# Kernel optimization log

Measured on AMD Instinct MI355X. Metric: run time of the kernel, lower is better.

## Reference

```python
import jax, jax.numpy as jnp
import numpy as np

N_EMBD = 2048
N_HEAD = 32
HEAD_SIZE = 64          # n_embd // n_head
MIX_DIM = 64            # RWKV-6 time-mix LoRA dim
DECAY_DIM = 128         # RWKV-6 decay LoRA dim
BATCH = 1024
STATE_ROWS = (2 + HEAD_SIZE) * 1  # single block, i = 0


def setup_inputs() -> dict:
    key = jax.random.key(0)
    ks = jax.random.split(key, 32)
    rn = lambda k, shp, s=0.02: jax.random.normal(k, shp, jnp.float32) * s
    d = {}
    d['x'] = jax.random.normal(ks[0], (BATCH, N_EMBD), jnp.float32)
    d['state'] = jax.random.normal(ks[1], (BATCH, STATE_ROWS, N_EMBD), jnp.float32) * 0.1
    d['ln1_w'] = jnp.ones((N_EMBD,), jnp.float32)
    d['ln1_b'] = jnp.zeros((N_EMBD,), jnp.float32)
    d['ln2_w'] = jnp.ones((N_EMBD,), jnp.float32)
    d['ln2_b'] = jnp.zeros((N_EMBD,), jnp.float32)
    d['maa_x'] = rn(ks[2], (N_EMBD,), 0.1)
    d['maa_w'] = rn(ks[3], (N_EMBD,), 0.1)
    d['maa_k'] = rn(ks[4], (N_EMBD,), 0.1)
    d['maa_v'] = rn(ks[5], (N_EMBD,), 0.1)
    d['maa_r'] = rn(ks[6], (N_EMBD,), 0.1)
    d['maa_g'] = rn(ks[7], (N_EMBD,), 0.1)
    d['maa_w1'] = rn(ks[8], (N_EMBD, 5 * MIX_DIM))
    d['maa_w2'] = rn(ks[9], (5, MIX_DIM, N_EMBD))
    d['decay'] = rn(ks[10], (N_EMBD,), 0.5) - 4.0  # typical negative log-decay
    d['decay_w1'] = rn(ks[11], (N_EMBD, DECAY_DIM))
    d['decay_w2'] = rn(ks[12], (DECAY_DIM, N_EMBD))
    d['faaaa'] = rn(ks[13], (N_HEAD, HEAD_SIZE, 1), 0.1)
    d['Wr'] = rn(ks[14], (N_EMBD, N_EMBD))
    d['Wk'] = rn(ks[15], (N_EMBD, N_EMBD))
    d['Wv'] = rn(ks[16], (N_EMBD, N_EMBD))
    d['Wo'] = rn(ks[17], (N_EMBD, N_EMBD))
    d['Wg'] = rn(ks[18], (N_EMBD, N_EMBD))
    d['gn_w'] = jnp.ones((N_EMBD,), jnp.float32)
    d['gn_b'] = jnp.zeros((N_EMBD,), jnp.float32)
    d['ffn_maa_k'] = rn(ks[19], (N_EMBD,), 0.1)
    d['ffn_maa_r'] = rn(ks[20], (N_EMBD,), 0.1)
    d['ffn_Wk'] = rn(ks[21], (N_EMBD, N_EMBD))
    d['ffn_Wr'] = rn(ks[22], (N_EMBD, N_EMBD))
    d['ffn_Wv'] = rn(ks[23], (N_EMBD, N_EMBD))
    d['i'] = 0
    return d


def _ln(x, w, b):
    mu = jnp.mean(x, -1, keepdims=True)
    var = jnp.var(x, -1, keepdims=True)
    return (x - mu) * jax.lax.rsqrt(var + 1e-5) * w + b


def reference(x, state, ln1_w, ln1_b, ln2_w, ln2_b,
              maa_x, maa_w, maa_k, maa_v, maa_r, maa_g, maa_w1, maa_w2,
              decay, decay_w1, decay_w2, faaaa,
              Wr, Wk, Wv, Wo, Wg, gn_w, gn_b,
              ffn_maa_k, ffn_maa_r, ffn_Wk, ffn_Wr, ffn_Wv, i):
    B = x.shape[0]
    H, S = N_HEAD, HEAD_SIZE
    # ---------------- time mixing ----------------
    xn = _ln(x, ln1_w, ln1_b)
    i1 = (2 + S) * i + 1
    sx = state[:, i1] - xn                                  # token shift delta
    xxx = xn + sx * maa_x
    xxx = jnp.tanh(xxx @ maa_w1).reshape(B, 5, 1, MIX_DIM)
    xxx = jnp.matmul(xxx, maa_w2).reshape(B, 5, N_EMBD)     # [B,5,E]
    mw, mk, mv, mr, mg = (xxx[:, j] for j in range(5))
    xw = xn + sx * (maa_w + mw)
    xk = xn + sx * (maa_k + mk)
    xv = xn + sx * (maa_v + mv)
    xr = xn + sx * (maa_r + mr)
    xg = xn + sx * (maa_g + mg)
    w = decay + jnp.tanh(xw @ decay_w1) @ decay_w2          # [B,E]
    w = jnp.exp(-jnp.exp(w.reshape(B, H, S, 1)))            # decay gate
    r = (xr @ Wr.T).reshape(B, H, 1, S)
    k = (xk @ Wk.T).reshape(B, H, S, 1)
    v = (xv @ Wv.T).reshape(B, H, 1, S)
    g = jax.nn.silu(xg @ Wg.T)
    s = state[:, (2 + S) * i + 2:(2 + S) * (i + 1), :].reshape(B, H, S, S)
    a = jnp.matmul(k, v)                                    # [B,H,S,S] outer product
    y = jnp.matmul(r, faaaa * a + s).reshape(B, N_EMBD)     # wkv readout
    # group norm (n_head groups over n_embd channels)
    yg = y.reshape(B, H, S)
    mu = jnp.mean(yg, -1, keepdims=True)
    var = jnp.var(yg, -1, keepdims=True)
    yg = ((yg - mu) * jax.lax.rsqrt(var + 1e-5)).reshape(B, N_EMBD) * gn_w + gn_b
    x1 = x + (yg * g) @ Wo.T
    # ---------------- channel mixing ----------------
    xn2 = _ln(x1, ln2_w, ln2_b)
    i0 = (2 + S) * i
    sx2 = state[:, i0] - xn2
    xk2 = xn2 + sx2 * ffn_maa_k
    xr2 = xn2 + sx2 * ffn_maa_r
    rr = jax.nn.sigmoid(xr2 @ ffn_Wr.T)
    kk = jnp.square(jax.nn.relu(xk2 @ ffn_Wk.T))
    return x1 + rr * (kk @ ffn_Wv.T)
```

## Files before the change

kernel.cpp:

```cpp
#include <hip/hip_runtime.h>
#include <cstdint>
#include <cstddef>

typedef unsigned short u16;
typedef __attribute__((ext_vector_type(8))) short bf16x8;
typedef __attribute__((ext_vector_type(4))) float f32x4;

#define DEV __device__ __forceinline__

DEV u16 f2bf(float f) {
  uint32_t b = __float_as_uint(f);
  b += 0x7fffu + ((b >> 16) & 1u);
  return (u16)(b >> 16);
}
DEV float bf2f(u16 u) { return __uint_as_float(((uint32_t)u) << 16); }

DEV void gl16(const u16* g, u16* l) {
  __builtin_amdgcn_global_load_lds(
      (const __attribute__((address_space(1))) void*)g,
      (__attribute__((address_space(3))) void*)l, 16, 0, 0);
}

struct CvtArgs { const float* s[8]; };

__global__ __launch_bounds__(256) void k_cvt_ln(
    const float* __restrict__ w1, const float* __restrict__ w2,
    u16* __restrict__ w1t, u16* __restrict__ w2t,
    const float* __restrict__ x, const float* __restrict__ state,
    const int* __restrict__ ip,
    const float* __restrict__ lw, const float* __restrict__ lb,
    const float* __restrict__ mx,
    u16* __restrict__ xn_o, u16* __restrict__ sx_o, u16* __restrict__ a1_o) {
  __shared__ float ls1[4], ls2[4];
  if (blockIdx.x < 4608) {
    int idx = blockIdx.x * 256 + threadIdx.x;
    if (idx < 655360) {
      int n = idx >> 11, k = idx & 2047;
      w1t[idx] = f2bf(w1[(size_t)k * 320 + n]);
    } else {
      int r = idx - 655360;
      int j = r >> 17, q = r & 131071;
      int n = q >> 6, k2 = q & 63;
      w2t[r] = f2bf(w2[((size_t)(j + 1) * 64 + k2) * 2048 + n]);
    }
  } else {
    int b = blockIdx.x - 4608, t = threadIdx.x;
    const float* xr = x + (size_t)b * 2048;
    float4 v0 = *(const float4*)(xr + t * 8);
    float4 v1 = *(const float4*)(xr + t * 8 + 4);
    float xv[8] = {v0.x, v0.y, v0.z, v0.w, v1.x, v1.y, v1.z, v1.w};
    float s1 = 0.f, s2 = 0.f;
#pragma unroll
    for (int j = 0; j < 8; ++j) { s1 += xv[j]; s2 += xv[j] * xv[j]; }
#pragma unroll
    for (int off = 32; off; off >>= 1) { s1 += __shfl_xor(s1, off); s2 += __shfl_xor(s2, off); }
    int w = t >> 6;
    if ((t & 63) == 0) { ls1[w] = s1; ls2[w] = s2; }
    __syncthreads();
    s1 = ls1[0] + ls1[1] + ls1[2] + ls1[3];
    s2 = ls2[0] + ls2[1] + ls2[2] + ls2[3];
    float mu = s1 * (1.0f / 2048.0f);
    float var = s2 * (1.0f / 2048.0f) - mu * mu;
    float rs = rsqrtf(var + 1e-5f);
    const float* st = state + ((size_t)b * 66 + (size_t)66 * ip[0] + 1) * 2048;
    int e0 = t * 8;
    uint4 xnp, sxp, a1p;
    u16* xnl = (u16*)&xnp; u16* sxl = (u16*)&sxp; u16* a1l = (u16*)&a1p;
#pragma unroll
    for (int j = 0; j < 8; ++j) {
      int e = e0 + j;
      float xn = (xv[j] - mu) * rs * lw[e] + lb[e];
      float sxv = st[e] - xn;
      xnl[j] = f2bf(xn); sxl[j] = f2bf(sxv); a1l[j] = f2bf(xn + sxv * mx[e]);
    }
    size_t o = (size_t)b * 2048 + e0;
    *(uint4*)(xn_o + o) = xnp;
    *(uint4*)(sx_o + o) = sxp;
    *(uint4*)(a1_o + o) = a1p;
  }
}

__global__ __launch_bounds__(256) void k_tanhpack(const float* __restrict__ p2,
                                                  u16* __restrict__ xb) {
  int idx = blockIdx.x * 256 + threadIdx.x;
  float s = p2[idx] + p2[327680 + idx] + p2[2 * 327680 + idx] + p2[3 * 327680 + idx];
  xb[idx] = f2bf(tanhf(s));
}

__global__ __launch_bounds__(256) void k_act(const u16* __restrict__ p8,
                                             u16* __restrict__ rr, u16* __restrict__ kk) {
  const size_t S = 2097152;
  int gid = blockIdx.x * 256 + threadIdx.x;
  size_t e0 = (size_t)(gid & 262143) * 8;
  int isk = gid >= 262144;
  const u16* base = p8 + (isk ? 4 * S : 0) + e0;
  float acc[8] = {};
#pragma unroll
  for (int s = 0; s < 4; ++s) {
    uint4 v = *(const uint4*)(base + (size_t)s * S);
    u16* vl = (u16*)&v;
#pragma unroll
    for (int j = 0; j < 8; ++j) acc[j] += bf2f(vl[j]);
  }
  uint4 p; u16* pl = (u16*)&p;
  if (!isk) {
#pragma unroll
    for (int j = 0; j < 8; ++j) pl[j] = f2bf(1.f / (1.f + __expf(-acc[j])));
    *(uint4*)(rr + e0) = p;
  } else {
#pragma unroll
    for (int j = 0; j < 8; ++j) { float r = acc[j] > 0.f ? acc[j] : 0.f; pl[j] = f2bf(r * r); }
    *(uint4*)(kk + e0) = p;
  }
}

__global__ __launch_bounds__(256) void k_fin(const u16* __restrict__ x1b,
                                             const u16* __restrict__ p9,
                                             const u16* __restrict__ rr,
                                             float* __restrict__ out) {
  const size_t S = 2097152;
  size_t e0 = ((size_t)blockIdx.x * 256 + threadIdx.x) * 8;
  float acc[8] = {};
#pragma unroll
  for (int s = 0; s < 4; ++s) {
    uint4 v = *(const uint4*)(p9 + (size_t)s * S + e0);
    u16* vl = (u16*)&v;
#pragma unroll
    for (int j = 0; j < 8; ++j) acc[j] += bf2f(vl[j]);
  }
  uint4 xv4 = *(const uint4*)(x1b + e0); u16* xl = (u16*)&xv4;
  uint4 rv = *(const uint4*)(rr + e0); u16* rl = (u16*)&rv;
  float o[8];
#pragma unroll
  for (int j = 0; j < 8; ++j) o[j] = bf2f(xl[j]) + bf2f(rl[j]) * acc[j];
  *(float4*)(out + e0) = make_float4(o[0], o[1], o[2], o[3]);
  *(float4*)(out + e0 + 4) = make_float4(o[4], o[5], o[6], o[7]);
}

__global__ __launch_bounds__(256) void k_ln_mix2(
    const float* __restrict__ x, const u16* __restrict__ p6,
    const float* __restrict__ state, const int* __restrict__ ip,
    const float* __restrict__ lw, const float* __restrict__ lb,
    const float* __restrict__ mk, const float* __restrict__ mr,
    u16* __restrict__ xk_o, u16* __restrict__ xr_o, u16* __restrict__ x1b_o) {
  const size_t S = 2097152;
  int b = blockIdx.x, t = threadIdx.x;
  size_t off = (size_t)b * 2048 + t * 8;
  float4 v0 = *(const float4*)(x + off);
  float4 v1 = *(const float4*)(x + off + 4);
  float xv[8] = {v0.x, v0.y, v0.z, v0.w, v1.x, v1.y, v1.z, v1.w};
#pragma unroll
  for (int s = 0; s < 4; ++s) {
    uint4 v = *(const uint4*)(p6 + (size_t)s * S + off);
    u16* vl = (u16*)&v;
#pragma unroll
    for (int j = 0; j < 8; ++j) xv[j] += bf2f(vl[j]);
  }
  uint4 x1p; u16* x1l = (u16*)&x1p;
#pragma unroll
  for (int j = 0; j < 8; ++j) x1l[j] = f2bf(xv[j]);
  *(uint4*)(x1b_o + off) = x1p;
  float s1 = 0.f, s2 = 0.f;
#pragma unroll
  for (int j = 0; j < 8; ++j) { s1 += xv[j]; s2 += xv[j] * xv[j]; }
#pragma unroll
  for (int off2 = 32; off2; off2 >>= 1) { s1 += __shfl_xor(s1, off2); s2 += __shfl_xor(s2, off2); }
  __shared__ float ls1[4], ls2[4];
  int w = t >> 6;
  if ((t & 63) == 0) { ls1[w] = s1; ls2[w] = s2; }
  __syncthreads();
  s1 = ls1[0] + ls1[1] + ls1[2] + ls1[3];
  s2 = ls2[0] + ls2[1] + ls2[2] + ls2[3];
  float mu = s1 * (1.0f / 2048.0f);
  float var = s2 * (1.0f / 2048.0f) - mu * mu;
  float rs = rsqrtf(var + 1e-5f);
  const float* st = state + ((size_t)b * 66 + (size_t)66 * ip[0] + 0) * 2048;
  int e0 = t * 8;
  uint4 xkp, xrp;
  u16* xkl = (u16*)&xkp; u16* xrl = (u16*)&xrp;
#pragma unroll
  for (int j = 0; j < 8; ++j) {
    int e = e0 + j;
    float xn = (xv[j] - mu) * rs * lw[e] + lb[e];
    float sxv = st[e] - xn;
    xkl[j] = f2bf(xn + sxv * mk[e]);
    xrl[j] = f2bf(xn + sxv * mr[e]);
  }
  *(uint4*)(xk_o + off) = xkp;
  *(uint4*)(xr_o + off) = xrp;
}

enum { EP_STORE = 0, EP_SILU, EP_MIX, EP_STOREF };

struct GemmDesc {
  const u16* A; const u16* B; void* C;
  const void* p1; const void* p2; const float* pvec;
  int lda, ldb, ldc, N, K, k0, ep;
};
struct GemmBatch { GemmDesc g[8]; int bpg; };

__global__ __launch_bounds__(256, 3) void k_gemmc(GemmBatch bat, int ngemm,
                                                  CvtArgs ca, u16* __restrict__ cdst,
                                                  int cvtoff) {
  if (blockIdx.x >= ngemm) {
    size_t idx = ((size_t)(blockIdx.x - ngemm + cvtoff) * 256 + threadIdx.x) * 8;
    int w = (int)(idx >> 22);
    size_t off = idx & ((1u << 22) - 1);
    const float* s = ca.s[w];
    float4 v0 = *(const float4*)(s + off);
    float4 v1 = *(const float4*)(s + off + 4);
    uint4 p; u16* pl = (u16*)&p;
    pl[0] = f2bf(v0.x); pl[1] = f2bf(v0.y); pl[2] = f2bf(v0.z); pl[3] = f2bf(v0.w);
    pl[4] = f2bf(v1.x); pl[5] = f2bf(v1.y); pl[6] = f2bf(v1.z); pl[7] = f2bf(v1.w);
    *(uint4*)(cdst + ((size_t)w << 22) + off) = p;
    return;
  }
  int gi = blockIdx.x / bat.bpg;
  int bid = blockIdx.x % bat.bpg;
  GemmDesc g = bat.g[gi];
  int ntn = (g.N + 127) >> 7;
  int m0 = (bid / ntn) << 7;
  int n0 = (bid % ntn) << 7;
  __shared__ u16 As[2][128 * 32];
  __shared__ u16 Bs[2][128 * 32];
  int t = threadIdx.x, w = t >> 6, lane = t & 63;
  int wm = w >> 1, wn = w & 1;
  int lr = lane & 15, kb = (lane >> 4) * 8;
  const u16* Ab = g.A + (size_t)(m0 + w * 32 + (lane >> 2)) * g.lda + (lane & 3) * 8;
  const u16* Bb = g.B + (size_t)(n0 + w * 32 + (lane >> 2)) * g.ldb + (lane & 3) * 8;
  int a16 = 16 * g.lda, b16 = 16 * g.ldb;
  int aoff = (w * 32) * 32;
  f32x4 acc[4][4] = {};
  int nt = g.K >> 5;

  auto stage = [&](int buf, int kk) {
    u16* Ad = (u16*)As + buf * 4096 + aoff;
    u16* Bd = (u16*)Bs + buf * 4096 + aoff;
    gl16(Ab + kk, Ad);
    gl16(Ab + kk + a16, Ad + 512);
    gl16(Bb + kk, Bd);
    gl16(Bb + kk + b16, Bd + 512);
  };

  stage(0, g.k0);
  __syncthreads();
  int cur = 0;
  for (int ti = 0; ti < nt; ++ti) {
    if (ti + 1 < nt) stage(cur ^ 1, g.k0 + (ti + 1) * 32);
    const u16* Ac = (const u16*)As + cur * 4096;
    const u16* Bc = (const u16*)Bs + cur * 4096;
    bf16x8 af[4], bfr[4];
#pragma unroll
    for (int m = 0; m < 4; ++m)
      af[m] = *(const bf16x8*)(Ac + (wm * 64 + m * 16 + lr) * 32 + kb);
#pragma unroll
    for (int n = 0; n < 4; ++n)
      bfr[n] = *(const bf16x8*)(Bc + (wn * 64 + n * 16 + lr) * 32 + kb);
#pragma unroll
    for (int m = 0; m < 4; ++m)
#pragma unroll
      for (int n = 0; n < 4; ++n)
        acc[m][n] = __builtin_amdgcn_mfma_f32_16x16x32_bf16(af[m], bfr[n], acc[m][n], 0, 0, 0);
    __syncthreads();
    cur ^= 1;
  }

  int ep = g.ep;
#pragma unroll
  for (int m = 0; m < 4; ++m) {
    int grow0 = m0 + wm * 64 + m * 16 + (lane >> 4) * 4;
#pragma unroll
    for (int n = 0; n < 4; ++n) {
      int gc = n0 + wn * 64 + n * 16 + lr;
      if (gc >= g.N) continue;
#pragma unroll
      for (int q = 0; q < 4; ++q) {
        size_t ci = (size_t)(grow0 + q) * g.ldc + gc;
        float v = acc[m][n][q];
        switch (ep) {
          case EP_STORE: ((u16*)g.C)[ci] = f2bf(v); break;
          case EP_MIX: {
            float xn = bf2f(((const u16*)g.p1)[ci]);
            float sxv = bf2f(((const u16*)g.p2)[ci]);
            ((u16*)g.C)[ci] = f2bf(xn + sxv * (g.pvec[gc] + v));
          } break;
          case EP_STOREF: ((float*)g.C)[ci] = v; break;
          default: break;
        }
      }
    }
  }
}

__global__ __launch_bounds__(512, 2) void k_gemm2(GemmBatch bat) {
  extern __shared__ u16 lds[];
  int nwg = gridDim.x;
  int wg0 = blockIdx.x;
  int wg = (wg0 & 7) * (nwg >> 3) + (wg0 >> 3);
  int gi = wg / bat.bpg;
  int bid = wg % bat.bpg;
  GemmDesc g = bat.g[gi];
  int ntn = (g.N + 255) >> 8;
  int m0 = (bid / ntn) << 7;
  int n0 = (bid % ntn) << 8;
  int t = threadIdx.x, wv = t >> 6, lane = t & 63;
  int wm = wv >> 2, wn = wv & 3;
  int lr = lane & 15, hi = lane >> 4;

  const u16* asrc[2]; const u16* bsrc[4];
#pragma unroll
  for (int j = 0; j < 2; ++j) {
    int cid = t + 512 * j, r = cid >> 3, c = cid & 7;
    asrc[j] = g.A + (size_t)(m0 + r) * g.lda + ((c ^ (r & 7)) << 3);
  }
#pragma unroll
  for (int j = 0; j < 4; ++j) {
    int cid = t + 512 * j, r = cid >> 3, c = cid & 7;
    bsrc[j] = g.B + (size_t)(n0 + r) * g.ldb + ((c ^ (r & 7)) << 3);
  }
  int au = wv * 512;

  auto stage = [&](int buf, int k) {
    u16* base = lds + buf * 24576;
#pragma unroll
    for (int j = 0; j < 2; ++j) gl16(asrc[j] + k, base + au + j * 4096);
#pragma unroll
    for (int j = 0; j < 4; ++j) gl16(bsrc[j] + k, base + 8192 + au + j * 4096);
  };

  int arow[4], brow[4];
#pragma unroll
  for (int m = 0; m < 4; ++m) arow[m] = wm * 64 + m * 16 + lr;
#pragma unroll
  for (int n = 0; n < 4; ++n) brow[n] = wn * 64 + n * 16 + lr;

  f32x4 acc[4][4] = {};
  int nt = g.K >> 6;
  stage(0, g.k0);
  if (nt > 1) stage(1, g.k0 + 64);

  for (int ti = 0; ti < nt; ++ti) {
    if (ti + 1 < nt) asm volatile("s_waitcnt vmcnt(6)" ::: "memory");
    else             asm volatile("s_waitcnt vmcnt(0)" ::: "memory");
    __builtin_amdgcn_sched_barrier(0);
    __builtin_amdgcn_s_barrier();
    __builtin_amdgcn_sched_barrier(0);
    const u16* buf = lds + (ti % 3) * 24576;
    bf16x8 af[4][2], bf[4][2];
#pragma unroll
    for (int m = 0; m < 4; ++m)
#pragma unroll
      for (int ks = 0; ks < 2; ++ks)
        af[m][ks] = *(const bf16x8*)(buf + arow[m] * 64 + ((((ks << 2) + hi) ^ (arow[m] & 7)) << 3));
#pragma unroll
    for (int n = 0; n < 4; ++n)
#pragma unroll
      for (int ks = 0; ks < 2; ++ks)
        bf[n][ks] = *(const bf16x8*)(buf + 8192 + brow[n] * 64 + ((((ks << 2) + hi) ^ (brow[n] & 7)) << 3));
    if (ti + 2 < nt) stage((ti + 2) % 3, g.k0 + (ti + 2) * 64);
    __builtin_amdgcn_s_setprio(1);
#pragma unroll
    for (int m = 0; m < 4; ++m)
#pragma unroll
      for (int n = 0; n < 4; ++n)
#pragma unroll
        for (int ks = 0; ks < 2; ++ks)
          acc[m][n] = __builtin_amdgcn_mfma_f32_16x16x32_bf16(af[m][ks], bf[n][ks], acc[m][n], 0, 0, 0);
    __builtin_amdgcn_s_setprio(0);
  }

  int ep = g.ep;
#pragma unroll
  for (int m = 0; m < 4; ++m) {
    int grow0 = m0 + wm * 64 + m * 16 + hi * 4;
#pragma unroll
    for (int n = 0; n < 4; ++n) {
      int gc = n0 + wn * 64 + n * 16 + lr;
#pragma unroll
      for (int q = 0; q < 4; ++q) {
        size_t ci = (size_t)(grow0 + q) * g.ldc + gc;
        float v = acc[m][n][q];
        switch (ep) {
          case EP_STORE: ((u16*)g.C)[ci] = f2bf(v); break;
          case EP_SILU:  ((u16*)g.C)[ci] = f2bf(v / (1.f + __expf(-v))); break;
          case EP_STOREF: ((float*)g.C)[ci] = v; break;
          default: break;
        }
      }
    }
  }
}

__global__ __launch_bounds__(512, 2) void k_gemm3(GemmBatch bat) {
  extern __shared__ u16 lds[];
  int nwg = gridDim.x;
  int wg0 = blockIdx.x;
  int wg = (wg0 & 7) * (nwg >> 3) + (wg0 >> 3);
  GemmDesc g = bat.g[wg / bat.bpg];
  int bid = wg % bat.bpg;
  int ntn = g.N >> 8;
  int m0 = (bid / ntn) << 8;
  int n0 = (bid % ntn) << 8;
  int t = threadIdx.x, wv = t >> 6, lane = t & 63;
  int wm = wv >> 2, wn = wv & 3;
  int lr = lane & 15, hi = lane >> 4;

  const u16* asrc[4]; const u16* bsrc[4];
#pragma unroll
  for (int j = 0; j < 4; ++j) {
    int cid = t + 512 * j, r = cid >> 3, c = cid & 7;
    asrc[j] = g.A + (size_t)(m0 + r) * g.lda + ((c ^ (r & 7)) << 3);
    bsrc[j] = g.B + (size_t)(n0 + r) * g.ldb + ((c ^ (r & 7)) << 3);
  }
  int au = wv * 512;

  auto stage = [&](int buf, int k) {
    u16* ab = lds + buf * 32768 + au;
    u16* bb = lds + buf * 32768 + 16384 + au;
#pragma unroll
    for (int j = 0; j < 4; ++j) gl16(asrc[j] + k, ab + j * 4096);
#pragma unroll
    for (int j = 0; j < 4; ++j) gl16(bsrc[j] + k, bb + j * 4096);
  };

  int arow[8], brow[4];
#pragma unroll
  for (int m = 0; m < 8; ++m) arow[m] = wm * 128 + m * 16 + lr;
#pragma unroll
  for (int n = 0; n < 4; ++n) brow[n] = wn * 64 + n * 16 + lr;

  f32x4 acc[8][4] = {};
  int nt = g.K >> 6;
  stage(0, g.k0);
  if (nt > 1) stage(1, g.k0 + 64);

  for (int ti = 0; ti < nt; ++ti) {
    if (ti + 1 < nt) asm volatile("s_waitcnt vmcnt(8)" ::: "memory");
    else             asm volatile("s_waitcnt vmcnt(0)" ::: "memory");
    __builtin_amdgcn_sched_barrier(0);
    __builtin_amdgcn_s_barrier();
    __builtin_amdgcn_sched_barrier(0);
    const u16* buf = lds + (ti & 1) * 32768;
#pragma unroll
    for (int ks = 0; ks < 2; ++ks) {
      bf16x8 af[8], bf[4];
#pragma unroll
      for (int m = 0; m < 8; ++m)
        af[m] = *(const bf16x8*)(buf + arow[m] * 64 + ((((ks << 2) + hi) ^ (arow[m] & 7)) << 3));
#pragma unroll
      for (int n = 0; n < 4; ++n)
        bf[n] = *(const bf16x8*)(buf + 16384 + brow[n] * 64 + ((((ks << 2) + hi) ^ (brow[n] & 7)) << 3));
      __builtin_amdgcn_s_setprio(1);
#pragma unroll
      for (int m = 0; m < 8; ++m)
#pragma unroll
        for (int n = 0; n < 4; ++n)
          acc[m][n] = __builtin_amdgcn_mfma_f32_16x16x32_bf16(af[m], bf[n], acc[m][n], 0, 0, 0);
      __builtin_amdgcn_s_setprio(0);
    }
    __builtin_amdgcn_sched_barrier(0);
    __builtin_amdgcn_s_barrier();
    __builtin_amdgcn_sched_barrier(0);
    if (ti + 2 < nt) stage(ti & 1, g.k0 + (ti + 2) * 64);
  }

#pragma unroll
  for (int m = 0; m < 8; ++m) {
    int grow0 = m0 + wm * 128 + m * 16 + hi * 4;
#pragma unroll
    for (int n = 0; n < 4; ++n) {
      int gc = n0 + wn * 64 + n * 16 + lr;
#pragma unroll
      for (int q = 0; q < 4; ++q)
        ((u16*)g.C)[(size_t)(grow0 + q) * g.ldc + gc] = f2bf(acc[m][n][q]);
    }
  }
}

__global__ __launch_bounds__(256) void k_wkv(
    const u16* __restrict__ p4,
    const float* __restrict__ state, const int* __restrict__ ip,
    const float* __restrict__ fa, const float* __restrict__ gw,
    const float* __restrict__ gbias, u16* __restrict__ t_o) {
  const size_t S = 2097152;
  int t = threadIdx.x, w = t >> 6, lane = t & 63;
  int flat = blockIdx.x * 4 + w;
  int b = flat >> 5, h = flat & 31;
  size_t base = ((size_t)b << 11) + (h << 6) + lane;
  float r  = bf2f(p4[base])         + bf2f(p4[S + base]);
  float kv = bf2f(p4[2 * S + base]) + bf2f(p4[3 * S + base]);
  float vv = bf2f(p4[4 * S + base]) + bf2f(p4[5 * S + base]);
  float gs = bf2f(p4[6 * S + base]) + bf2f(p4[7 * S + base]);
  float gg = gs / (1.f + __expf(-gs));
  float f  = fa[(h << 6) + lane];
  __shared__ float rs[4][64];
  rs[w][lane] = r;
  __syncthreads();
  float c = r * f * kv;
#pragma unroll
  for (int off = 32; off; off >>= 1) c += __shfl_xor(c, off);

  const float* sp = state + ((size_t)b * 66 + (size_t)66 * ip[0] + 2 + 2 * h) * 2048;
  int q = lane >> 4, jj = lane & 15;
  float yp0 = 0.f, yp1 = 0.f, yp2 = 0.f, yp3 = 0.f;
#pragma unroll
  for (int ib = 0; ib < 16; ++ib) {
    int i = ib * 4 + q;
    float4 sv = *(const float4*)(sp + ((i >> 5) * 2048) + ((i & 31) << 6) + jj * 4);
    float ri = rs[w][i];
    yp0 += ri * sv.x; yp1 += ri * sv.y; yp2 += ri * sv.z; yp3 += ri * sv.w;
  }
#pragma unroll
  for (int off = 16; off <= 32; off <<= 1) {
    yp0 += __shfl_xor(yp0, off); yp1 += __shfl_xor(yp1, off);
    yp2 += __shfl_xor(yp2, off); yp3 += __shfl_xor(yp3, off);
  }
  int src = lane >> 2, cc = lane & 3;
  float t0 = __shfl(yp0, src), t1 = __shfl(yp1, src);
  float t2 = __shfl(yp2, src), t3 = __shfl(yp3, src);
  float y = cc == 0 ? t0 : cc == 1 ? t1 : cc == 2 ? t2 : t3;
  y += c * vv;
  float s1 = y, s2 = y * y;
#pragma unroll
  for (int off = 32; off; off >>= 1) { s1 += __shfl_xor(s1, off); s2 += __shfl_xor(s2, off); }
  float mu = s1 * (1.f / 64.f);
  float var = s2 * (1.f / 64.f) - mu * mu;
  float yn = (y - mu) * rsqrtf(var + 1e-5f);
  float tg = (yn * gw[(h << 6) + lane] + gbias[(h << 6) + lane]) * gg;
  t_o[((size_t)b << 11) + (h << 6) + lane] = f2bf(tg);
}

extern "C" void kernel_launch(void* const* d_in, const int* in_sizes, int n_in,
                              void* d_out, int out_size, void* d_ws, size_t ws_size,
                              hipStream_t stream) {
  const float* x      = (const float*)d_in[0];
  const float* state  = (const float*)d_in[1];
  const float* ln1_w  = (const float*)d_in[2];
  const float* ln1_b  = (const float*)d_in[3];
  const float* ln2_w  = (const float*)d_in[4];
  const float* ln2_b  = (const float*)d_in[5];
  const float* maa_x  = (const float*)d_in[6];
  const float* maa_k  = (const float*)d_in[8];
  const float* maa_v  = (const float*)d_in[9];
  const float* maa_r  = (const float*)d_in[10];
  const float* maa_g  = (const float*)d_in[11];
  const float* maa_w1 = (const float*)d_in[12];
  const float* maa_w2 = (const float*)d_in[13];
  const float* faaaa  = (const float*)d_in[17];
  const float* Wr     = (const float*)d_in[18];
  const float* Wk     = (const float*)d_in[19];
  const float* Wv     = (const float*)d_in[20];
  const float* Wo     = (const float*)d_in[21];
  const float* Wg     = (const float*)d_in[22];
  const float* gn_w   = (const float*)d_in[23];
  const float* gn_b   = (const float*)d_in[24];
  const float* fmk    = (const float*)d_in[25];
  const float* fmr    = (const float*)d_in[26];
  const float* fWk    = (const float*)d_in[27];
  const float* fWr    = (const float*)d_in[28];
  const float* fWv    = (const float*)d_in[29];
  const int*   ip     = (const int*)d_in[30];
  float* out = (float*)d_out;

  char* wsb = (char*)d_ws;
  const size_t MB = 1ull << 20;
  u16* wbf   = (u16*)(wsb + 0 * MB);
  u16* w1t   = (u16*)(wsb + 64 * MB);
  u16* w2t   = (u16*)(wsb + 66 * MB);
  u16* xn    = (u16*)(wsb + 68 * MB);
  u16* sx    = (u16*)(wsb + 72 * MB);
  u16* a1    = (u16*)(wsb + 76 * MB);
  float* p2  = (float*)(wsb + 80 * MB);
  u16* xxx   = (u16*)(wsb + 86 * MB);
  u16* xk    = (u16*)(wsb + 87 * MB);
  u16* xv    = (u16*)(wsb + 91 * MB);
  u16* xr    = (u16*)(wsb + 95 * MB);
  u16* xg    = (u16*)(wsb + 99 * MB);
  u16* p4    = (u16*)(wsb + 103 * MB);
  u16* tb    = (u16*)(wsb + 135 * MB);
  u16* p6    = (u16*)(wsb + 139 * MB);
  u16* x1b   = (u16*)(wsb + 155 * MB);
  u16* xk2   = (u16*)(wsb + 159 * MB);
  u16* xr2   = (u16*)(wsb + 163 * MB);
  u16* p8    = (u16*)(wsb + 167 * MB);
  u16* rr    = (u16*)(wsb + 199 * MB);
  u16* kkb   = (u16*)(wsb + 203 * MB);
  u16* p9    = (u16*)(wsb + 207 * MB);

  const size_t WSQ = 4194304, S = 2097152;
  u16* bWr = wbf + 0 * WSQ; u16* bWk = wbf + 1 * WSQ; u16* bWv = wbf + 2 * WSQ;
  u16* bWg = wbf + 3 * WSQ; u16* bWo = wbf + 4 * WSQ; u16* bfWr = wbf + 5 * WSQ;
  u16* bfWk = wbf + 6 * WSQ; u16* bfWv = wbf + 7 * WSQ;

  auto mkd = [](const u16* A, const u16* B, void* C, const void* p1,
                const void* p2_, const float* pvec, int lda, int ldb, int ldc,
                int N, int K, int k0, int epf) {
    GemmDesc d; d.A = A; d.B = B; d.C = C; d.p1 = p1; d.p2 = p2_; d.pvec = pvec;
    d.lda = lda; d.ldb = ldb; d.ldc = ldc; d.N = N; d.K = K; d.k0 = k0; d.ep = epf;
    return d;
  };

  CvtArgs ca; ca.s[0] = Wr; ca.s[1] = Wk; ca.s[2] = Wv; ca.s[3] = Wg;
  ca.s[4] = Wo; ca.s[5] = fWr; ca.s[6] = fWk; ca.s[7] = fWv;

  static const int LDS2 = 147456;
  static const int LDS3 = 131072;
  hipFuncSetAttribute((const void*)k_gemm2,
                      hipFuncAttributeMaxDynamicSharedMemorySize, LDS2);
  hipFuncSetAttribute((const void*)k_gemm3,
                      hipFuncAttributeMaxDynamicSharedMemorySize, LDS3);

  k_cvt_ln<<<5632, 256, 0, stream>>>(maa_w1, maa_w2, w1t, w2t,
                                     x, state, ip, ln1_w, ln1_b, maa_x, xn, sx, a1);

  {
    GemmBatch g{}; g.bpg = 8 * 3;
    for (int j = 0; j < 4; ++j)
      g.g[j] = mkd(a1, w1t, p2 + (size_t)j * 327680, nullptr, nullptr, nullptr,
                   2048, 2048, 320, 320, 512, j * 512, EP_STOREF);
    k_gemmc<<<96 + 8192, 256, 0, stream>>>(g, 96, ca, wbf, 0);
  }
  k_tanhpack<<<1280, 256, 0, stream>>>(p2, xxx);

  {
    GemmBatch g{}; g.bpg = 8 * 16;
    const float* mv[4] = {maa_k, maa_v, maa_r, maa_g};
    u16* tv[4] = {xk, xv, xr, xg};
    for (int j = 1; j <= 4; ++j)
      g.g[j - 1] = mkd(xxx + j * 64, w2t + (size_t)(j - 1) * 131072, tv[j - 1],
                       xn, sx, mv[j - 1], 320, 64, 2048, 2048, 64, 0, EP_MIX);
    k_gemmc<<<512 + 8192, 256, 0, stream>>>(g, 512, ca, wbf, 8192);
  }

  {
    GemmBatch g{}; g.bpg = 32;
    const u16* av[4] = {xr, xk, xv, xg};
    const u16* bv[4] = {bWr, bWk, bWv, bWg};
    for (int q = 0; q < 4; ++q)
      for (int s = 0; s < 2; ++s)
        g.g[q * 2 + s] = mkd(av[q], bv[q], p4 + (size_t)(q * 2 + s) * S,
                             nullptr, nullptr, nullptr, 2048, 2048, 2048,
                             2048, 1024, s * 1024, EP_STORE);
    k_gemm3<<<256, 512, LDS3, stream>>>(g);
  }

  k_wkv<<<8192, 256, 0, stream>>>(p4, state, ip, faaaa, gn_w, gn_b, tb);

  {
    GemmBatch g{}; g.bpg = 8 * 8;
    for (int s = 0; s < 4; ++s)
      g.g[s] = mkd(tb, bWo, p6 + (size_t)s * S, nullptr, nullptr, nullptr,
                   2048, 2048, 2048, 2048, 512, s * 512, EP_STORE);
    k_gemm2<<<256, 512, LDS2, stream>>>(g);
  }

  k_ln_mix2<<<1024, 256, 0, stream>>>(x, p6, state, ip, ln2_w, ln2_b, fmk, fmr,
                                      xk2, xr2, x1b);

  {
    GemmBatch g{}; g.bpg = 32;
    for (int s = 0; s < 4; ++s) {
      g.g[s]     = mkd(xr2, bfWr, p8 + (size_t)s * S, nullptr, nullptr, nullptr,
                       2048, 2048, 2048, 2048, 512, s * 512, EP_STORE);
      g.g[4 + s] = mkd(xk2, bfWk, p8 + (size_t)(4 + s) * S, nullptr, nullptr, nullptr,
                       2048, 2048, 2048, 2048, 512, s * 512, EP_STORE);
    }
    k_gemm3<<<256, 512, LDS3, stream>>>(g);
  }
  k_act<<<2048, 256, 0, stream>>>(p8, rr, kkb);

  {
    GemmBatch g{}; g.bpg = 8 * 8;
    for (int s = 0; s < 4; ++s)
      g.g[s] = mkd(kkb, bfWv, p9 + (size_t)s * S, nullptr, nullptr, nullptr,
                   2048, 2048, 2048, 2048, 512, s * 512, EP_STORE);
    k_gemm2<<<256, 512, LDS2, stream>>>(g);
  }

  k_fin<<<1024, 256, 0, stream>>>(x1b, p9, rr, out);
}
```

Baseline: 319.7 us.

## Replace split-K gemm3 with gemm2 full-K tiles and fuse SiLU epilogue

```diff
diff --git a/kernel.cpp b/kernel.cpp
--- a/kernel.cpp
+++ b/kernel.cpp
@@ -93,10 +93,10 @@
   int gid = blockIdx.x * 256 + threadIdx.x;
   size_t e0 = (size_t)(gid & 262143) * 8;
   int isk = gid >= 262144;
-  const u16* base = p8 + (isk ? 4 * S : 0) + e0;
+  const u16* base = p8 + (isk ? 2 * S : 0) + e0;
   float acc[8] = {};
 #pragma unroll
-  for (int s = 0; s < 4; ++s) {
+  for (int s = 0; s < 2; ++s) {
     uint4 v = *(const uint4*)(base + (size_t)s * S);
     u16* vl = (u16*)&v;
 #pragma unroll
@@ -391,107 +391,20 @@
   }
 }
 
-__global__ __launch_bounds__(512, 2) void k_gemm3(GemmBatch bat) {
-  extern __shared__ u16 lds[];
-  int nwg = gridDim.x;
-  int wg0 = blockIdx.x;
-  int wg = (wg0 & 7) * (nwg >> 3) + (wg0 >> 3);
-  GemmDesc g = bat.g[wg / bat.bpg];
-  int bid = wg % bat.bpg;
-  int ntn = g.N >> 8;
-  int m0 = (bid / ntn) << 8;
-  int n0 = (bid % ntn) << 8;
-  int t = threadIdx.x, wv = t >> 6, lane = t & 63;
-  int wm = wv >> 2, wn = wv & 3;
-  int lr = lane & 15, hi = lane >> 4;
-
-  const u16* asrc[4]; const u16* bsrc[4];
-#pragma unroll
-  for (int j = 0; j < 4; ++j) {
-    int cid = t + 512 * j, r = cid >> 3, c = cid & 7;
-    asrc[j] = g.A + (size_t)(m0 + r) * g.lda + ((c ^ (r & 7)) << 3);
-    bsrc[j] = g.B + (size_t)(n0 + r) * g.ldb + ((c ^ (r & 7)) << 3);
-  }
-  int au = wv * 512;
-
-  auto stage = [&](int buf, int k) {
-    u16* ab = lds + buf * 32768 + au;
-    u16* bb = lds + buf * 32768 + 16384 + au;
-#pragma unroll
-    for (int j = 0; j < 4; ++j) gl16(asrc[j] + k, ab + j * 4096);
-#pragma unroll
-    for (int j = 0; j < 4; ++j) gl16(bsrc[j] + k, bb + j * 4096);
-  };
-
-  int arow[8], brow[4];
-#pragma unroll
-  for (int m = 0; m < 8; ++m) arow[m] = wm * 128 + m * 16 + lr;
-#pragma unroll
-  for (int n = 0; n < 4; ++n) brow[n] = wn * 64 + n * 16 + lr;
-
-  f32x4 acc[8][4] = {};
-  int nt = g.K >> 6;
-  stage(0, g.k0);
-  if (nt > 1) stage(1, g.k0 + 64);
-
-  for (int ti = 0; ti < nt; ++ti) {
-    if (ti + 1 < nt) asm volatile("s_waitcnt vmcnt(8)" ::: "memory");
-    else             asm volatile("s_waitcnt vmcnt(0)" ::: "memory");
-    __builtin_amdgcn_sched_barrier(0);
-    __builtin_amdgcn_s_barrier();
-    __builtin_amdgcn_sched_barrier(0);
-    const u16* buf = lds + (ti & 1) * 32768;
-#pragma unroll
-    for (int ks = 0; ks < 2; ++ks) {
-      bf16x8 af[8], bf[4];
-#pragma unroll
-      for (int m = 0; m < 8; ++m)
-        af[m] = *(const bf16x8*)(buf + arow[m] * 64 + ((((ks << 2) + hi) ^ (arow[m] & 7)) << 3));
-#pragma unroll
-      for (int n = 0; n < 4; ++n)
-        bf[n] = *(const bf16x8*)(buf + 16384 + brow[n] * 64 + ((((ks << 2) + hi) ^ (brow[n] & 7)) << 3));
-      __builtin_amdgcn_s_setprio(1);
-#pragma unroll
-      for (int m = 0; m < 8; ++m)
-#pragma unroll
-        for (int n = 0; n < 4; ++n)
-          acc[m][n] = __builtin_amdgcn_mfma_f32_16x16x32_bf16(af[m], bf[n], acc[m][n], 0, 0, 0);
-      __builtin_amdgcn_s_setprio(0);
-    }
-    __builtin_amdgcn_sched_barrier(0);
-    __builtin_amdgcn_s_barrier();
-    __builtin_amdgcn_sched_barrier(0);
-    if (ti + 2 < nt) stage(ti & 1, g.k0 + (ti + 2) * 64);
-  }
-
-#pragma unroll
-  for (int m = 0; m < 8; ++m) {
-    int grow0 = m0 + wm * 128 + m * 16 + hi * 4;
-#pragma unroll
-    for (int n = 0; n < 4; ++n) {
-      int gc = n0 + wn * 64 + n * 16 + lr;
-#pragma unroll
-      for (int q = 0; q < 4; ++q)
-        ((u16*)g.C)[(size_t)(grow0 + q) * g.ldc + gc] = f2bf(acc[m][n][q]);
-    }
-  }
-}
-
 __global__ __launch_bounds__(256) void k_wkv(
-    const u16* __restrict__ p4,
+    const u16* __restrict__ rb, const u16* __restrict__ kb,
+    const u16* __restrict__ vb, const u16* __restrict__ gb,
     const float* __restrict__ state, const int* __restrict__ ip,
     const float* __restrict__ fa, const float* __restrict__ gw,
     const float* __restrict__ gbias, u16* __restrict__ t_o) {
-  const size_t S = 2097152;
   int t = threadIdx.x, w = t >> 6, lane = t & 63;
   int flat = blockIdx.x * 4 + w;
   int b = flat >> 5, h = flat & 31;
   size_t base = ((size_t)b << 11) + (h << 6) + lane;
-  float r  = bf2f(p4[base])         + bf2f(p4[S + base]);
-  float kv = bf2f(p4[2 * S + base]) + bf2f(p4[3 * S + base]);
-  float vv = bf2f(p4[4 * S + base]) + bf2f(p4[5 * S + base]);
-  float gs = bf2f(p4[6 * S + base]) + bf2f(p4[7 * S + base]);
-  float gg = gs / (1.f + __expf(-gs));
+  float r  = bf2f(rb[base]);
+  float kv = bf2f(kb[base]);
+  float vv = bf2f(vb[base]);
+  float gg = bf2f(gb[base]);
   float f  = fa[(h << 6) + lane];
   __shared__ float rs[4][64];
   rs[w][lane] = r;
@@ -527,7 +440,7 @@
   float var = s2 * (1.f / 64.f) - mu * mu;
   float yn = (y - mu) * rsqrtf(var + 1e-5f);
   float tg = (yn * gw[(h << 6) + lane] + gbias[(h << 6) + lane]) * gg;
-  t_o[((size_t)b << 11) + (h << 6) + lane] = f2bf(tg);
+  t_o[base] = f2bf(tg);
 }
 
 extern "C" void kernel_launch(void* const* d_in, const int* in_sizes, int n_in,
@@ -576,16 +489,19 @@
   u16* xv    = (u16*)(wsb + 91 * MB);
   u16* xr    = (u16*)(wsb + 95 * MB);
   u16* xg    = (u16*)(wsb + 99 * MB);
-  u16* p4    = (u16*)(wsb + 103 * MB);
-  u16* tb    = (u16*)(wsb + 135 * MB);
-  u16* p6    = (u16*)(wsb + 139 * MB);
-  u16* x1b   = (u16*)(wsb + 155 * MB);
-  u16* xk2   = (u16*)(wsb + 159 * MB);
-  u16* xr2   = (u16*)(wsb + 163 * MB);
-  u16* p8    = (u16*)(wsb + 167 * MB);
-  u16* rr    = (u16*)(wsb + 199 * MB);
-  u16* kkb   = (u16*)(wsb + 203 * MB);
-  u16* p9    = (u16*)(wsb + 207 * MB);
+  u16* rb    = (u16*)(wsb + 103 * MB);
+  u16* kb    = (u16*)(wsb + 107 * MB);
+  u16* vb    = (u16*)(wsb + 111 * MB);
+  u16* gb    = (u16*)(wsb + 115 * MB);
+  u16* tb    = (u16*)(wsb + 119 * MB);
+  u16* p6    = (u16*)(wsb + 123 * MB);
+  u16* x1b   = (u16*)(wsb + 139 * MB);
+  u16* xk2   = (u16*)(wsb + 143 * MB);
+  u16* xr2   = (u16*)(wsb + 147 * MB);
+  u16* p8    = (u16*)(wsb + 151 * MB);
+  u16* rr    = (u16*)(wsb + 167 * MB);
+  u16* kkb   = (u16*)(wsb + 171 * MB);
+  u16* p9    = (u16*)(wsb + 175 * MB);
 
   const size_t WSQ = 4194304, S = 2097152;
   u16* bWr = wbf + 0 * WSQ; u16* bWk = wbf + 1 * WSQ; u16* bWv = wbf + 2 * WSQ;
@@ -604,11 +520,8 @@
   ca.s[4] = Wo; ca.s[5] = fWr; ca.s[6] = fWk; ca.s[7] = fWv;
 
   static const int LDS2 = 147456;
-  static const int LDS3 = 131072;
   hipFuncSetAttribute((const void*)k_gemm2,
                       hipFuncAttributeMaxDynamicSharedMemorySize, LDS2);
-  hipFuncSetAttribute((const void*)k_gemm3,
-                      hipFuncAttributeMaxDynamicSharedMemorySize, LDS3);
 
   k_cvt_ln<<<5632, 256, 0, stream>>>(maa_w1, maa_w2, w1t, w2t,
                                      x, state, ip, ln1_w, ln1_b, maa_x, xn, sx, a1);
@@ -633,18 +546,15 @@
   }
 
   {
-    GemmBatch g{}; g.bpg = 32;
-    const u16* av[4] = {xr, xk, xv, xg};
-    const u16* bv[4] = {bWr, bWk, bWv, bWg};
-    for (int q = 0; q < 4; ++q)
-      for (int s = 0; s < 2; ++s)
-        g.g[q * 2 + s] = mkd(av[q], bv[q], p4 + (size_t)(q * 2 + s) * S,
-                             nullptr, nullptr, nullptr, 2048, 2048, 2048,
-                             2048, 1024, s * 1024, EP_STORE);
-    k_gemm3<<<256, 512, LDS3, stream>>>(g);
-  }
-
-  k_wkv<<<8192, 256, 0, stream>>>(p4, state, ip, faaaa, gn_w, gn_b, tb);
+    GemmBatch g{}; g.bpg = 8 * 8;
+    g.g[0] = mkd(xr, bWr, rb, nullptr, nullptr, nullptr, 2048, 2048, 2048, 2048, 2048, 0, EP_STORE);
+    g.g[1] = mkd(xk, bWk, kb, nullptr, nullptr, nullptr, 2048, 2048, 2048, 2048, 2048, 0, EP_STORE);
+    g.g[2] = mkd(xv, bWv, vb, nullptr, nullptr, nullptr, 2048, 2048, 2048, 2048, 2048, 0, EP_STORE);
+    g.g[3] = mkd(xg, bWg, gb, nullptr, nullptr, nullptr, 2048, 2048, 2048, 2048, 2048, 0, EP_SILU);
+    k_gemm2<<<256, 512, LDS2, stream>>>(g);
+  }
+
+  k_wkv<<<8192, 256, 0, stream>>>(rb, kb, vb, gb, state, ip, faaaa, gn_w, gn_b, tb);
 
   {
     GemmBatch g{}; g.bpg = 8 * 8;
@@ -658,14 +568,14 @@
                                       xk2, xr2, x1b);
 
   {
-    GemmBatch g{}; g.bpg = 32;
-    for (int s = 0; s < 4; ++s) {
+    GemmBatch g{}; g.bpg = 8 * 8;
+    for (int s = 0; s < 2; ++s) {
       g.g[s]     = mkd(xr2, bfWr, p8 + (size_t)s * S, nullptr, nullptr, nullptr,
-                       2048, 2048, 2048, 2048, 512, s * 512, EP_STORE);
-      g.g[4 + s] = mkd(xk2, bfWk, p8 + (size_t)(4 + s) * S, nullptr, nullptr, nullptr,
-                       2048, 2048, 2048, 2048, 512, s * 512, EP_STORE);
+                       2048, 2048, 2048, 2048, 1024, s * 1024, EP_STORE);
+      g.g[2 + s] = mkd(xk2, bfWk, p8 + (size_t)(2 + s) * S, nullptr, nullptr, nullptr,
+                       2048, 2048, 2048, 2048, 1024, s * 1024, EP_STORE);
     }
-    k_gemm3<<<256, 512, LDS3, stream>>>(g);
+    k_gemm2<<<256, 512, LDS2, stream>>>(g);
   }
   k_act<<<2048, 256, 0, stream>>>(p8, rr, kkb);
 
```

New measurement: 310.9 us (median of 3 runs). 2.8% less time.

## Replace 256x256 GEMM with 128x256 triple-buffered kernel and rebalance split-K

Applied to the files above, without the earlier changes.

```diff
diff --git a/kernel.cpp b/kernel.cpp
--- a/kernel.cpp
+++ b/kernel.cpp
@@ -93,10 +93,10 @@
   int gid = blockIdx.x * 256 + threadIdx.x;
   size_t e0 = (size_t)(gid & 262143) * 8;
   int isk = gid >= 262144;
-  const u16* base = p8 + (isk ? 4 * S : 0) + e0;
+  const u16* base = p8 + (isk ? 2 * S : 0) + e0;
   float acc[8] = {};
 #pragma unroll
-  for (int s = 0; s < 4; ++s) {
+  for (int s = 0; s < 2; ++s) {
     uint4 v = *(const uint4*)(base + (size_t)s * S);
     u16* vl = (u16*)&v;
 #pragma unroll
@@ -391,82 +391,73 @@
   }
 }
 
-__global__ __launch_bounds__(512, 2) void k_gemm3(GemmBatch bat) {
+__global__ __launch_bounds__(512, 4) void k_gemm2b(GemmBatch bat) {
   extern __shared__ u16 lds[];
   int nwg = gridDim.x;
   int wg0 = blockIdx.x;
   int wg = (wg0 & 7) * (nwg >> 3) + (wg0 >> 3);
   GemmDesc g = bat.g[wg / bat.bpg];
   int bid = wg % bat.bpg;
-  int ntn = g.N >> 8;
-  int m0 = (bid / ntn) << 8;
+  int ntn = (g.N + 255) >> 8;
+  int m0 = (bid / ntn) << 7;
   int n0 = (bid % ntn) << 8;
   int t = threadIdx.x, wv = t >> 6, lane = t & 63;
   int wm = wv >> 2, wn = wv & 3;
   int lr = lane & 15, hi = lane >> 4;
 
-  const u16* asrc[4]; const u16* bsrc[4];
-#pragma unroll
-  for (int j = 0; j < 4; ++j) {
-    int cid = t + 512 * j, r = cid >> 3, c = cid & 7;
-    asrc[j] = g.A + (size_t)(m0 + r) * g.lda + ((c ^ (r & 7)) << 3);
-    bsrc[j] = g.B + (size_t)(n0 + r) * g.ldb + ((c ^ (r & 7)) << 3);
-  }
+  int r = t >> 2, c = t & 3;
+  int cc = ((c ^ ((r >> 1) & 3)) << 3);
+  const u16* asrc  = g.A + (size_t)(m0 + r) * g.lda + cc;
+  const u16* bsrc0 = g.B + (size_t)(n0 + r) * g.ldb + cc;
+  const u16* bsrc1 = g.B + (size_t)(n0 + 128 + r) * g.ldb + cc;
   int au = wv * 512;
 
   auto stage = [&](int buf, int k) {
-    u16* ab = lds + buf * 32768 + au;
-    u16* bb = lds + buf * 32768 + 16384 + au;
-#pragma unroll
-    for (int j = 0; j < 4; ++j) gl16(asrc[j] + k, ab + j * 4096);
-#pragma unroll
-    for (int j = 0; j < 4; ++j) gl16(bsrc[j] + k, bb + j * 4096);
+    u16* base = lds + buf * 12288;
+    gl16(asrc + k, base + au);
+    gl16(bsrc0 + k, base + 4096 + au);
+    gl16(bsrc1 + k, base + 8192 + au);
   };
 
-  int arow[8], brow[4];
-#pragma unroll
-  for (int m = 0; m < 8; ++m) arow[m] = wm * 128 + m * 16 + lr;
+  int arow[4], brow[4];
+#pragma unroll
+  for (int m = 0; m < 4; ++m) arow[m] = wm * 64 + m * 16 + lr;
 #pragma unroll
   for (int n = 0; n < 4; ++n) brow[n] = wn * 64 + n * 16 + lr;
-
-  f32x4 acc[8][4] = {};
-  int nt = g.K >> 6;
+  int swz = ((hi ^ ((lr >> 1) & 3)) << 3);
+
+  f32x4 acc[4][4] = {};
+  int nt = g.K >> 5;
   stage(0, g.k0);
-  if (nt > 1) stage(1, g.k0 + 64);
+  if (nt > 1) stage(1, g.k0 + 32);
 
   for (int ti = 0; ti < nt; ++ti) {
-    if (ti + 1 < nt) asm volatile("s_waitcnt vmcnt(8)" ::: "memory");
+    if (ti + 1 < nt) asm volatile("s_waitcnt vmcnt(3)" ::: "memory");
     else             asm volatile("s_waitcnt vmcnt(0)" ::: "memory");
     __builtin_amdgcn_sched_barrier(0);
     __builtin_amdgcn_s_barrier();
     __builtin_amdgcn_sched_barrier(0);
-    const u16* buf = lds + (ti & 1) * 32768;
-#pragma unroll
-    for (int ks = 0; ks < 2; ++ks) {
-      bf16x8 af[8], bf[4];
-#pragma unroll
-      for (int m = 0; m < 8; ++m)
-        af[m] = *(const bf16x8*)(buf + arow[m] * 64 + ((((ks << 2) + hi) ^ (arow[m] & 7)) << 3));
+    const u16* buf = lds + (ti % 3) * 12288;
+    bf16x8 af[4], bfr[4];
+#pragma unroll
+    for (int m = 0; m < 4; ++m)
+      af[m] = *(const bf16x8*)(buf + arow[m] * 32 + swz);
+#pragma unroll
+    for (int n = 0; n < 4; ++n)
+      bfr[n] = *(const bf16x8*)(buf + 4096 + brow[n] * 32 + swz);
+    if (ti + 2 < nt) stage((ti + 2) % 3, g.k0 + (ti + 2) * 32);
+    __builtin_amdgcn_s_setprio(1);
+#pragma unroll
+    for (int m = 0; m < 4; ++m)
 #pragma unroll
       for (int n = 0; n < 4; ++n)
-        bf[n] = *(const bf16x8*)(buf + 16384 + brow[n] * 64 + ((((ks << 2) + hi) ^ (brow[n] & 7)) << 3));
-      __builtin_amdgcn_s_setprio(1);
-#pragma unroll
-      for (int m = 0; m < 8; ++m)
-#pragma unroll
-        for (int n = 0; n < 4; ++n)
-          acc[m][n] = __builtin_amdgcn_mfma_f32_16x16x32_bf16(af[m], bf[n], acc[m][n], 0, 0, 0);
-      __builtin_amdgcn_s_setprio(0);
-    }
-    __builtin_amdgcn_sched_barrier(0);
-    __builtin_amdgcn_s_barrier();
-    __builtin_amdgcn_sched_barrier(0);
-    if (ti + 2 < nt) stage(ti & 1, g.k0 + (ti + 2) * 64);
-  }
-
-#pragma unroll
-  for (int m = 0; m < 8; ++m) {
-    int grow0 = m0 + wm * 128 + m * 16 + hi * 4;
+        acc[m][n] = __builtin_amdgcn_mfma_f32_16x16x32_bf16(af[m], bfr[n], acc[m][n], 0, 0, 0);
+    __builtin_amdgcn_s_setprio(0);
+  }
+
+#pragma unroll
+  for (int m = 0; m < 4; ++m) {
+    int grow0 = m0 + wm * 64 + m * 16 + hi * 4;
 #pragma unroll
     for (int n = 0; n < 4; ++n) {
       int gc = n0 + wn * 64 + n * 16 + lr;
@@ -527,7 +518,7 @@
   float var = s2 * (1.f / 64.f) - mu * mu;
   float yn = (y - mu) * rsqrtf(var + 1e-5f);
   float tg = (yn * gw[(h << 6) + lane] + gbias[(h << 6) + lane]) * gg;
-  t_o[((size_t)b << 11) + (h << 6) + lane] = f2bf(tg);
+  t_o[base] = f2bf(tg);
 }
 
 extern "C" void kernel_launch(void* const* d_in, const int* in_sizes, int n_in,
@@ -583,9 +574,9 @@
   u16* xk2   = (u16*)(wsb + 159 * MB);
   u16* xr2   = (u16*)(wsb + 163 * MB);
   u16* p8    = (u16*)(wsb + 167 * MB);
-  u16* rr    = (u16*)(wsb + 199 * MB);
-  u16* kkb   = (u16*)(wsb + 203 * MB);
-  u16* p9    = (u16*)(wsb + 207 * MB);
+  u16* rr    = (u16*)(wsb + 183 * MB);
+  u16* kkb   = (u16*)(wsb + 187 * MB);
+  u16* p9    = (u16*)(wsb + 191 * MB);
 
   const size_t WSQ = 4194304, S = 2097152;
   u16* bWr = wbf + 0 * WSQ; u16* bWk = wbf + 1 * WSQ; u16* bWv = wbf + 2 * WSQ;
@@ -603,12 +594,12 @@
   CvtArgs ca; ca.s[0] = Wr; ca.s[1] = Wk; ca.s[2] = Wv; ca.s[3] = Wg;
   ca.s[4] = Wo; ca.s[5] = fWr; ca.s[6] = fWk; ca.s[7] = fWv;
 
-  static const int LDS2 = 147456;
-  static const int LDS3 = 131072;
+  static const int LDS2  = 147456;
+  static const int LDS2B = 73728;
   hipFuncSetAttribute((const void*)k_gemm2,
                       hipFuncAttributeMaxDynamicSharedMemorySize, LDS2);
-  hipFuncSetAttribute((const void*)k_gemm3,
-                      hipFuncAttributeMaxDynamicSharedMemorySize, LDS3);
+  hipFuncSetAttribute((const void*)k_gemm2b,
+                      hipFuncAttributeMaxDynamicSharedMemorySize, LDS2B);
 
   k_cvt_ln<<<5632, 256, 0, stream>>>(maa_w1, maa_w2, w1t, w2t,
                                      x, state, ip, ln1_w, ln1_b, maa_x, xn, sx, a1);
@@ -633,7 +624,7 @@
   }
 
   {
-    GemmBatch g{}; g.bpg = 32;
+    GemmBatch g{}; g.bpg = 64;
     const u16* av[4] = {xr, xk, xv, xg};
     const u16* bv[4] = {bWr, bWk, bWv, bWg};
     for (int q = 0; q < 4; ++q)
@@ -641,7 +632,7 @@
         g.g[q * 2 + s] = mkd(av[q], bv[q], p4 + (size_t)(q * 2 + s) * S,
                              nullptr, nullptr, nullptr, 2048, 2048, 2048,
                              2048, 1024, s * 1024, EP_STORE);
-    k_gemm3<<<256, 512, LDS3, stream>>>(g);
+    k_gemm2b<<<512, 512, LDS2B, stream>>>(g);
   }
 
   k_wkv<<<8192, 256, 0, stream>>>(p4, state, ip, faaaa, gn_w, gn_b, tb);
@@ -658,14 +649,14 @@
                                       xk2, xr2, x1b);
 
   {
-    GemmBatch g{}; g.bpg = 32;
-    for (int s = 0; s < 4; ++s) {
+    GemmBatch g{}; g.bpg = 8 * 8;
+    for (int s = 0; s < 2; ++s) {
       g.g[s]     = mkd(xr2, bfWr, p8 + (size_t)s * S, nullptr, nullptr, nullptr,
-                       2048, 2048, 2048, 2048, 512, s * 512, EP_STORE);
-      g.g[4 + s] = mkd(xk2, bfWk, p8 + (size_t)(4 + s) * S, nullptr, nullptr, nullptr,
-                       2048, 2048, 2048, 2048, 512, s * 512, EP_STORE);
+                       2048, 2048, 2048, 2048, 1024, s * 1024, EP_STORE);
+      g.g[2 + s] = mkd(xk2, bfWk, p8 + (size_t)(2 + s) * S, nullptr, nullptr, nullptr,
+                       2048, 2048, 2048, 2048, 1024, s * 1024, EP_STORE);
     }
-    k_gemm3<<<256, 512, LDS3, stream>>>(g);
+    k_gemm2<<<256, 512, LDS2, stream>>>(g);
   }
   k_act<<<2048, 256, 0, stream>>>(p8, rr, kkb);
 
```

Measured after the change: 317.4 us. Within noise of the previous version (-0.7%).
